# Kernel optimization log

Measured on AMD Instinct MI355X. Metric: run time of the kernel, lower is better.

## Reference

```python
import jax, jax.numpy as jnp
import numpy as np

WINDOW = 50


def setup_inputs() -> dict:
    key = jax.random.key(0)
    ks = jax.random.split(key, 7)
    B, N = 32, 32768
    hidden = 32
    x = jax.random.normal(ks[0], (B, N), dtype=jnp.float32)
    # torch Linear weights stored as [in, out] (already transposed)
    w1 = jax.random.normal(ks[1], (4, 2 * hidden), dtype=jnp.float32) * (1.0 / np.sqrt(4))
    b1 = jnp.zeros((2 * hidden,), dtype=jnp.float32)
    w2 = jax.random.normal(ks[2], (2 * hidden, hidden), dtype=jnp.float32) * (1.0 / np.sqrt(2 * hidden))
    b2 = jnp.zeros((hidden,), dtype=jnp.float32)
    w3 = jax.random.normal(ks[3], (hidden, 2), dtype=jnp.float32) * (1.0 / np.sqrt(hidden))
    b3 = jnp.zeros((2,), dtype=jnp.float32)
    return {"x": x, "w1": w1, "b1": b1, "w2": w2, "b2": b2, "w3": w3, "b3": b3}


def reference(x, w1, b1, w2, b2, w3, b3):
    W = WINDOW
    B, N = x.shape
    M = N - W + 1
    # windows: [B, M, W] via gather (same layout as torch.unfold)
    idx = jnp.arange(M)[:, None] + jnp.arange(W)[None, :]  # [M, W]
    windows = x[:, idx]  # [B, M, W]
    mean = windows.mean(axis=-1, keepdims=True)
    centered = windows - mean
    # torch .std() is unbiased (ddof=1)
    var = (centered ** 2).sum(axis=-1, keepdims=True) / (W - 1)
    std = jnp.sqrt(var) + 1e-6
    skew = (centered ** 3).mean(axis=-1, keepdims=True) / std ** 3
    kurt = (centered ** 4).mean(axis=-1, keepdims=True) / std ** 4
    stats = jnp.concatenate([mean, std, skew, kurt], axis=-1)  # [B, M, 4]
    h = jax.nn.relu(stats @ w1 + b1)
    h = jax.nn.relu(h @ w2 + b2)
    params = h @ w3 + b3  # [B, M, 2]
    gamma = params[:, :, 0:1]
    beta = params[:, :, 1:2]
    normalized = centered / std
    reprojected = normalized * gamma + beta  # [B, M, W]
    return reprojected[:, :, W // 2]  # [B, M]
```

## Files before the change

### kernel.cpp

```cpp
#include <hip/hip_runtime.h>
#include <hip/hip_bf16.h>
#include <math.h>

#define WINDOW 50
#define BPT 256

typedef __attribute__((ext_vector_type(8))) short short8;
typedef __attribute__((ext_vector_type(4))) float f32x4;
typedef unsigned int uint;

union U8 { uint4 u; short8 s; };
__device__ inline short8 as_s8(uint4 u) { U8 t; t.u = u; return t.s; }

__device__ inline uint pk2(float a, float b) {
    uint r;
    asm("v_cvt_pk_bf16_f32 %0, %1, %2" : "=v"(r) : "v"(a), "v"(b));
    return r;
}
__device__ inline float lo_f32(uint u) { return __uint_as_float(u << 16); }
__device__ inline float hi_f32(uint u) { return __uint_as_float(u & 0xffff0000u); }

#define LDS_FENCE() do { asm volatile("s_waitcnt lgkmcnt(0)" ::: "memory"); \
                         __builtin_amdgcn_sched_barrier(0); } while (0)

__global__ __launch_bounds__(256) void nsg_kernel(
    const float* __restrict__ x,
    const float* __restrict__ w1, const float* __restrict__ b1,
    const float* __restrict__ w2, const float* __restrict__ b2,
    const float* __restrict__ w3, const float* __restrict__ b3,
    float* __restrict__ out, int B, int N, int M, int tiles)
{
    __shared__ float s_x[BPT + WINDOW + 2];
    __shared__ f32x4 s_chunk[BPT + 40];
    __shared__ uint4 s_stat[4][64];
    __shared__ uint4 s_h1[4][128];
    __shared__ f32x4 s_h2[4][512];
    __shared__ f32x4 s_b1q[16];
    __shared__ f32x4 s_b2q[8];

    const int tid  = threadIdx.x;
    const int wv   = tid >> 6;
    const int wl   = tid & 63;
    const int l15  = wl & 15;
    const int g    = wl >> 4;
    const int tile = blockIdx.x % tiles;
    const int row  = blockIdx.x / tiles;
    const int m0   = tile * BPT;

    const float* xr = x + (size_t)row * N;
    for (int i = tid; i < BPT + WINDOW; i += 256) {
        int gg = m0 + i;
        s_x[i] = (gg < N) ? xr[gg] : 0.0f;
    }
    if (tid < 16) s_b1q[tid] = ((const f32x4*)b1)[tid];
    if (tid < 8)  s_b2q[tid] = ((const f32x4*)b2)[tid];

    short8 A1[4];
    #pragma unroll
    for (int nt = 0; nt < 4; ++nt) {
        int n = nt * 16 + l15;
        float a = w1[0 * 64 + n], b = w1[1 * 64 + n];
        float c = w1[2 * 64 + n], d = w1[3 * 64 + n];
        uint hab = pk2(a, b), hcd = pk2(c, d);
        float la = a - lo_f32(hab), lb = b - hi_f32(hab);
        float lc = c - lo_f32(hcd), ld = d - hi_f32(hcd);
        uint lab = pk2(la, lb), lcd = pk2(lc, ld);
        uint4 u;
        if (g == 0)      u = make_uint4(hab, hcd, hab, hcd);
        else if (g == 1) u = make_uint4(lab, lcd, lab, lcd);
        else             u = make_uint4(0, 0, 0, 0);
        A1[nt] = as_s8(u);
    }
    short8 A2h[2][2], A2l[2][2];
    #pragma unroll
    for (int mt = 0; mt < 2; ++mt) {
        int c = mt * 16 + l15;
        #pragma unroll
        for (int ks = 0; ks < 2; ++ks) {
            uint hu[4], lu[4];
            #pragma unroll
            for (int p = 0; p < 4; ++p) {
                int n = ks * 32 + g * 8 + 2 * p;
                float a = w2[n * 32 + c], b = w2[(n + 1) * 32 + c];
                uint h = pk2(a, b);
                float la = a - lo_f32(h), lb = b - hi_f32(h);
                hu[p] = h; lu[p] = pk2(la, lb);
            }
            A2h[mt][ks] = as_s8(make_uint4(hu[0], hu[1], hu[2], hu[3]));
            A2l[mt][ks] = as_s8(make_uint4(lu[0], lu[1], lu[2], lu[3]));
        }
    }
    __syncthreads();

    f32x4 myC;
    {
        float S1 = 0.f, S2 = 0.f, S3 = 0.f, S4 = 0.f;
        #pragma unroll
        for (int i = 0; i < 10; ++i) {
            float v = s_x[tid + i], v2 = v * v;
            S1 += v; S2 += v2; S3 = fmaf(v2, v, S3); S4 = fmaf(v2, v2, S4);
        }
        myC = f32x4{S1, S2, S3, S4};
        s_chunk[tid] = myC;
    }
    if (tid < 40) {
        float S1 = 0.f, S2 = 0.f, S3 = 0.f, S4 = 0.f;
        #pragma unroll
        for (int i = 0; i < 10; ++i) {
            float v = s_x[256 + tid + i], v2 = v * v;
            S1 += v; S2 += v2; S3 = fmaf(v2, v, S3); S4 = fmaf(v2, v2, S4);
        }
        s_chunk[256 + tid] = f32x4{S1, S2, S3, S4};
    }
    __syncthreads();

    f32x4 ca = s_chunk[tid + 10], cb = s_chunk[tid + 20];
    f32x4 cc = s_chunk[tid + 30], cd = s_chunk[tid + 40];
    float S1 = myC[0] + ca[0] + cb[0] + cc[0] + cd[0];
    float S2 = myC[1] + ca[1] + cb[1] + cc[1] + cd[1];
    float S3 = myC[2] + ca[2] + cb[2] + cc[2] + cd[2];
    float S4 = myC[3] + ca[3] + cb[3] + cc[3] + cd[3];

    const float invW = 1.0f / (float)WINDOW;
    float mean = S1 * invW;
    float mu2  = mean * mean;
    float c2m = S2 - (float)WINDOW * mu2;
    float c3m = S3 - 3.0f * mean * S2 + 2.0f * (float)WINDOW * mu2 * mean;
    float c4m = S4 - 4.0f * mean * S3 + 6.0f * mu2 * S2
                  - 3.0f * (float)WINDOW * mu2 * mu2;
    float var    = c2m * (1.0f / (float)(WINDOW - 1));
    float sd     = sqrtf(var) + 1e-6f;
    float inv_sd = 1.0f / sd;
    float inv_sd2 = inv_sd * inv_sd;
    float skew = c3m * invW * inv_sd2 * inv_sd;
    float kurt = c4m * invW * inv_sd2 * inv_sd2;
    float center = s_x[tid + 25];

    {
        uint h01 = pk2(mean, sd), h23 = pk2(skew, kurt);
        float ml = mean - lo_f32(h01), sl = sd   - hi_f32(h01);
        float kl = skew - lo_f32(h23), ul = kurt - hi_f32(h23);
        uint l01 = pk2(ml, sl), l23 = pk2(kl, ul);
        s_stat[wv][wl] = make_uint4(h01, h23, l01, l23);
    }
    LDS_FENCE();

    uint2* ph1 = (uint2*)&s_h1[wv][0];

    #pragma unroll
    for (int wt = 0; wt < 4; ++wt) {
        int w = wt * 16 + l15;
        short8 B1 = as_s8(s_stat[wv][w]);

        f32x4 C1[4];
        #pragma unroll
        for (int nt = 0; nt < 4; ++nt) C1[nt] = s_b1q[nt * 4 + g];
        #pragma unroll
        for (int nt = 0; nt < 4; ++nt)
            C1[nt] = __builtin_amdgcn_mfma_f32_16x16x32_bf16(A1[nt], B1, C1[nt], 0, 0, 0);

        #pragma unroll
        for (int nt = 0; nt < 4; ++nt) {
            uint p01 = pk2(fmaxf(C1[nt][0], 0.f), fmaxf(C1[nt][1], 0.f));
            uint p23 = pk2(fmaxf(C1[nt][2], 0.f), fmaxf(C1[nt][3], 0.f));
            int q = nt * 4 + g;
            uint2 t; t.x = p01; t.y = p23;
            ph1[(l15 * 16 + q) ^ ((l15 & 7) << 1)] = t;
        }
        LDS_FENCE();

        short8 B2k0 = as_s8(s_h1[wv][(l15 * 8 + 0 + g) ^ (l15 & 7)]);
        short8 B2k1 = as_s8(s_h1[wv][(l15 * 8 + 4 + g) ^ (l15 & 7)]);

        f32x4 C2[2];
        #pragma unroll
        for (int mt = 0; mt < 2; ++mt) C2[mt] = s_b2q[mt * 4 + g];
        #pragma unroll
        for (int mt = 0; mt < 2; ++mt) {
            C2[mt] = __builtin_amdgcn_mfma_f32_16x16x32_bf16(A2h[mt][0], B2k0, C2[mt], 0, 0, 0);
            C2[mt] = __builtin_amdgcn_mfma_f32_16x16x32_bf16(A2h[mt][1], B2k1, C2[mt], 0, 0, 0);
            C2[mt] = __builtin_amdgcn_mfma_f32_16x16x32_bf16(A2l[mt][0], B2k0, C2[mt], 0, 0, 0);
            C2[mt] = __builtin_amdgcn_mfma_f32_16x16x32_bf16(A2l[mt][1], B2k1, C2[mt], 0, 0, 0);
        }
        #pragma unroll
        for (int mt = 0; mt < 2; ++mt) {
            f32x4 hq;
            #pragma unroll
            for (int j = 0; j < 4; ++j) hq[j] = fmaxf(C2[mt][j], 0.f);
            s_h2[wv][(w * 8 + mt * 4 + g) ^ (w & 7)] = hq;
        }
    }
    LDS_FENCE();

    float gam = b3[0], bet = b3[1];
    #pragma unroll
    for (int q = 0; q < 8; ++q) {
        f32x4 h = s_h2[wv][(wl * 8 + q) ^ (wl & 7)];
        #pragma unroll
        for (int j = 0; j < 4; ++j) {
            int c = 16 * (q >> 2) + 4 * (q & 3) + j;
            gam = fmaf(h[j], w3[c * 2 + 0], gam);
            bet = fmaf(h[j], w3[c * 2 + 1], bet);
        }
    }

    const int m = m0 + tid;
    if (m < M)
        out[(size_t)row * M + m] = fmaf((center - mean) * inv_sd, gam, bet);
}

extern "C" void kernel_launch(void* const* d_in, const int* in_sizes, int n_in,
                              void* d_out, int out_size, void* d_ws, size_t ws_size,
                              hipStream_t stream) {
    const float* x  = (const float*)d_in[0];
    const float* w1 = (const float*)d_in[1];
    const float* b1 = (const float*)d_in[2];
    const float* w2 = (const float*)d_in[3];
    const float* b2 = (const float*)d_in[4];
    const float* w3 = (const float*)d_in[5];
    const float* b3 = (const float*)d_in[6];
    float* out = (float*)d_out;

    const int N = 32768;
    const int B = in_sizes[0] / N;
    const int M = N - WINDOW + 1;
    const int tiles = (M + BPT - 1) / BPT;

    dim3 grid(B * tiles), block(BPT);
    nsg_kernel<<<grid, block, 0, stream>>>(x, w1, b1, w2, b2, w3, b3,
                                           out, B, N, M, tiles);
}
```

Baseline: 35.63 us.

## Process two outputs per thread and fuse MLP layer-3 into MFMA epilogue

Each block now covers 512 output positions with 256 threads, so each thread handles two windows and the per-block weight-setup cost is amortized. The layer-1 bias is folded into the MFMA via a ones-row in B, and the layer-1 activation is split into hi/lo bf16 parts for extra precision. The A2 low part moves to LDS to cut register pressure, and launch bounds request 4 blocks per CU. The h2 store to LDS and the serial w3 dot product are replaced by an in-register reduction with cross-lane shuffles, at the cost of more MFMAs per tile and halving the grid size.

```diff
diff --git a/kernel.cpp b/kernel.cpp
--- a/kernel.cpp
+++ b/kernel.cpp
@@ -3,7 +3,6 @@
 #include <math.h>
 
 #define WINDOW 50
-#define BPT 256
 
 typedef __attribute__((ext_vector_type(8))) short short8;
 typedef __attribute__((ext_vector_type(4))) float f32x4;
@@ -20,58 +19,53 @@
 __device__ inline float lo_f32(uint u) { return __uint_as_float(u << 16); }
 __device__ inline float hi_f32(uint u) { return __uint_as_float(u & 0xffff0000u); }
 
-#define LDS_FENCE() do { asm volatile("s_waitcnt lgkmcnt(0)" ::: "memory"); \
-                         __builtin_amdgcn_sched_barrier(0); } while (0)
-
-__global__ __launch_bounds__(256) void nsg_kernel(
+__global__ __launch_bounds__(256, 4) void nsg_kernel(
     const float* __restrict__ x,
     const float* __restrict__ w1, const float* __restrict__ b1,
     const float* __restrict__ w2, const float* __restrict__ b2,
     const float* __restrict__ w3, const float* __restrict__ b3,
-    float* __restrict__ out, int B, int N, int M, int tiles)
+    float* __restrict__ out, int N, int M, int tiles)
 {
-    __shared__ float s_x[BPT + WINDOW + 2];
-    __shared__ f32x4 s_chunk[BPT + 40];
-    __shared__ uint4 s_stat[4][64];
-    __shared__ uint4 s_h1[4][128];
-    __shared__ f32x4 s_h2[4][512];
-    __shared__ f32x4 s_b1q[16];
-    __shared__ f32x4 s_b2q[8];
-
-    const int tid  = threadIdx.x;
-    const int wv   = tid >> 6;
-    const int wl   = tid & 63;
-    const int l15  = wl & 15;
-    const int g    = wl >> 4;
+    __shared__ float s_x[564];
+    __shared__ f32x4 s_buf[1088];
+    __shared__ uint4 s_a2l[4][64];
+    __shared__ uint4 s_stat[4][128];
+
+    const int tid = threadIdx.x;
+    const int wv  = tid >> 6;
+    const int wl  = tid & 63;
+    const int l15 = wl & 15;
+    const int g   = wl >> 4;
     const int tile = blockIdx.x % tiles;
     const int row  = blockIdx.x / tiles;
-    const int m0   = tile * BPT;
+    const int m0   = tile * 512;
 
     const float* xr = x + (size_t)row * N;
-    for (int i = tid; i < BPT + WINDOW; i += 256) {
+    for (int i = tid; i < 562; i += 256) {
         int gg = m0 + i;
         s_x[i] = (gg < N) ? xr[gg] : 0.0f;
     }
-    if (tid < 16) s_b1q[tid] = ((const f32x4*)b1)[tid];
-    if (tid < 8)  s_b2q[tid] = ((const f32x4*)b2)[tid];
 
     short8 A1[4];
     #pragma unroll
     for (int nt = 0; nt < 4; ++nt) {
         int n = nt * 16 + l15;
-        float a = w1[0 * 64 + n], b = w1[1 * 64 + n];
-        float c = w1[2 * 64 + n], d = w1[3 * 64 + n];
+        float a = w1[n], b = w1[64 + n], c = w1[128 + n], d = w1[192 + n];
         uint hab = pk2(a, b), hcd = pk2(c, d);
-        float la = a - lo_f32(hab), lb = b - hi_f32(hab);
-        float lc = c - lo_f32(hcd), ld = d - hi_f32(hcd);
-        uint lab = pk2(la, lb), lcd = pk2(lc, ld);
+        uint lab = pk2(a - lo_f32(hab), b - hi_f32(hab));
+        uint lcd = pk2(c - lo_f32(hcd), d - hi_f32(hcd));
+        float bb = b1[n];
+        uint bh = pk2(bb, 0.0f);
+        uint bpk = pk2(bb, bb - lo_f32(bh));
         uint4 u;
-        if (g == 0)      u = make_uint4(hab, hcd, hab, hcd);
-        else if (g == 1) u = make_uint4(lab, lcd, lab, lcd);
-        else             u = make_uint4(0, 0, 0, 0);
+        u.x = (g == 0) ? hab : (g == 1) ? lab : (g == 2) ? bpk : 0u;
+        u.y = (g == 0) ? hcd : (g == 1) ? lcd : 0u;
+        u.z = (g == 0) ? hab : (g == 1) ? lab : 0u;
+        u.w = (g == 0) ? hcd : (g == 1) ? lcd : 0u;
         A1[nt] = as_s8(u);
     }
-    short8 A2h[2][2], A2l[2][2];
+
+    uint4 A2h[2][2];
     #pragma unroll
     for (int mt = 0; mt < 2; ++mt) {
         int c = mt * 16 + l15;
@@ -83,130 +77,154 @@
                 int n = ks * 32 + g * 8 + 2 * p;
                 float a = w2[n * 32 + c], b = w2[(n + 1) * 32 + c];
                 uint h = pk2(a, b);
-                float la = a - lo_f32(h), lb = b - hi_f32(h);
-                hu[p] = h; lu[p] = pk2(la, lb);
+                hu[p] = h;
+                lu[p] = pk2(a - lo_f32(h), b - hi_f32(h));
             }
-            A2h[mt][ks] = as_s8(make_uint4(hu[0], hu[1], hu[2], hu[3]));
-            A2l[mt][ks] = as_s8(make_uint4(lu[0], lu[1], lu[2], lu[3]));
-        }
-    }
+            A2h[mt][ks] = make_uint4(hu[0], hu[1], hu[2], hu[3]);
+            if (wv == 0) s_a2l[mt * 2 + ks][wl] = make_uint4(lu[0], lu[1], lu[2], lu[3]);
+        }
+    }
+
+    f32x4 b2r[2];
+    #pragma unroll
+    for (int mt = 0; mt < 2; ++mt)
+        b2r[mt] = *(const f32x4*)(b2 + 16 * mt + 4 * g);
+    float2 w3r[8];
+    #pragma unroll
+    for (int mt = 0; mt < 2; ++mt)
+        #pragma unroll
+        for (int j = 0; j < 4; ++j)
+            w3r[mt * 4 + j] = *(const float2*)(w3 + (16 * mt + 4 * g + j) * 2);
+    const float b3g = b3[0], b3b = b3[1];
+
     __syncthreads();
 
-    f32x4 myC;
-    {
+    f32x4* s_chunk = s_buf;
+    f32x4 myC[2];
+    #pragma unroll
+    for (int s = 0; s < 2; ++s) {
+        int t = tid + 256 * s;
         float S1 = 0.f, S2 = 0.f, S3 = 0.f, S4 = 0.f;
         #pragma unroll
         for (int i = 0; i < 10; ++i) {
-            float v = s_x[tid + i], v2 = v * v;
+            float v = s_x[t + i], v2 = v * v;
             S1 += v; S2 += v2; S3 = fmaf(v2, v, S3); S4 = fmaf(v2, v2, S4);
         }
-        myC = f32x4{S1, S2, S3, S4};
-        s_chunk[tid] = myC;
+        myC[s] = f32x4{S1, S2, S3, S4};
+        s_chunk[t] = myC[s];
     }
     if (tid < 40) {
+        int t = tid + 512;
         float S1 = 0.f, S2 = 0.f, S3 = 0.f, S4 = 0.f;
         #pragma unroll
         for (int i = 0; i < 10; ++i) {
-            float v = s_x[256 + tid + i], v2 = v * v;
+            float v = s_x[t + i], v2 = v * v;
             S1 += v; S2 += v2; S3 = fmaf(v2, v, S3); S4 = fmaf(v2, v2, S4);
         }
-        s_chunk[256 + tid] = f32x4{S1, S2, S3, S4};
+        s_chunk[t] = f32x4{S1, S2, S3, S4};
     }
     __syncthreads();
 
-    f32x4 ca = s_chunk[tid + 10], cb = s_chunk[tid + 20];
-    f32x4 cc = s_chunk[tid + 30], cd = s_chunk[tid + 40];
-    float S1 = myC[0] + ca[0] + cb[0] + cc[0] + cd[0];
-    float S2 = myC[1] + ca[1] + cb[1] + cc[1] + cd[1];
-    float S3 = myC[2] + ca[2] + cb[2] + cc[2] + cd[2];
-    float S4 = myC[3] + ca[3] + cb[3] + cc[3] + cd[3];
-
-    const float invW = 1.0f / (float)WINDOW;
-    float mean = S1 * invW;
-    float mu2  = mean * mean;
-    float c2m = S2 - (float)WINDOW * mu2;
-    float c3m = S3 - 3.0f * mean * S2 + 2.0f * (float)WINDOW * mu2 * mean;
-    float c4m = S4 - 4.0f * mean * S3 + 6.0f * mu2 * S2
-                  - 3.0f * (float)WINDOW * mu2 * mu2;
-    float var    = c2m * (1.0f / (float)(WINDOW - 1));
-    float sd     = sqrtf(var) + 1e-6f;
-    float inv_sd = 1.0f / sd;
-    float inv_sd2 = inv_sd * inv_sd;
-    float skew = c3m * invW * inv_sd2 * inv_sd;
-    float kurt = c4m * invW * inv_sd2 * inv_sd2;
-    float center = s_x[tid + 25];
-
-    {
+    float nrm[2];
+    #pragma unroll
+    for (int s = 0; s < 2; ++s) {
+        int t = tid + 256 * s;
+        f32x4 ca = s_chunk[t + 10], cb = s_chunk[t + 20];
+        f32x4 cc = s_chunk[t + 30], cd = s_chunk[t + 40];
+        float S1 = myC[s][0] + ca[0] + cb[0] + cc[0] + cd[0];
+        float S2 = myC[s][1] + ca[1] + cb[1] + cc[1] + cd[1];
+        float S3 = myC[s][2] + ca[2] + cb[2] + cc[2] + cd[2];
+        float S4 = myC[s][3] + ca[3] + cb[3] + cc[3] + cd[3];
+        const float invW = 1.0f / (float)WINDOW;
+        float mean = S1 * invW;
+        float mu2  = mean * mean;
+        float c2m = S2 - (float)WINDOW * mu2;
+        float c3m = S3 - 3.0f * mean * S2 + 2.0f * (float)WINDOW * mu2 * mean;
+        float c4m = S4 - 4.0f * mean * S3 + 6.0f * mu2 * S2
+                      - 3.0f * (float)WINDOW * mu2 * mu2;
+        float var    = c2m * (1.0f / (float)(WINDOW - 1));
+        float sd     = sqrtf(var) + 1e-6f;
+        float inv_sd = 1.0f / sd;
+        float inv_sd2 = inv_sd * inv_sd;
+        float skew = c3m * invW * inv_sd2 * inv_sd;
+        float kurt = c4m * invW * inv_sd2 * inv_sd2;
         uint h01 = pk2(mean, sd), h23 = pk2(skew, kurt);
-        float ml = mean - lo_f32(h01), sl = sd   - hi_f32(h01);
-        float kl = skew - lo_f32(h23), ul = kurt - hi_f32(h23);
-        uint l01 = pk2(ml, sl), l23 = pk2(kl, ul);
-        s_stat[wv][wl] = make_uint4(h01, h23, l01, l23);
-    }
-    LDS_FENCE();
-
-    uint2* ph1 = (uint2*)&s_h1[wv][0];
-
-    #pragma unroll
-    for (int wt = 0; wt < 4; ++wt) {
-        int w = wt * 16 + l15;
-        short8 B1 = as_s8(s_stat[wv][w]);
-
-        f32x4 C1[4];
-        #pragma unroll
-        for (int nt = 0; nt < 4; ++nt) C1[nt] = s_b1q[nt * 4 + g];
-        #pragma unroll
-        for (int nt = 0; nt < 4; ++nt)
-            C1[nt] = __builtin_amdgcn_mfma_f32_16x16x32_bf16(A1[nt], B1, C1[nt], 0, 0, 0);
+        uint l01 = pk2(mean - lo_f32(h01), sd - hi_f32(h01));
+        uint l23 = pk2(skew - lo_f32(h23), kurt - hi_f32(h23));
+        s_stat[wv][s * 64 + wl] = make_uint4(h01, h23, l01, l23);
+        nrm[s] = (s_x[t + 25] - mean) * inv_sd;
+    }
+    __syncthreads();
+
+    uint* h1b = (uint*)(s_buf + wv * 272);
+    const uint K2 = (g == 2) ? 0x3F803F80u : 0u;
+    const bool gHi = (g >= 2);
+    float ga[2] = {0.f, 0.f}, be[2] = {0.f, 0.f};
+
+    #pragma unroll
+    for (int q = 0; q < 8; ++q) {
+        const int s = q >> 2, sub = q & 3;
+        uint4 st = s_stat[wv][s * 64 + sub * 16 + l15];
+        uint4 bq;
+        bq.x = gHi ? K2 : st.x;
+        bq.y = gHi ? 0u : st.y;
+        bq.z = gHi ? 0u : st.z;
+        bq.w = gHi ? 0u : st.w;
+        short8 B1 = as_s8(bq);
 
         #pragma unroll
         for (int nt = 0; nt < 4; ++nt) {
-            uint p01 = pk2(fmaxf(C1[nt][0], 0.f), fmaxf(C1[nt][1], 0.f));
-            uint p23 = pk2(fmaxf(C1[nt][2], 0.f), fmaxf(C1[nt][3], 0.f));
-            int q = nt * 4 + g;
-            uint2 t; t.x = p01; t.y = p23;
-            ph1[(l15 * 16 + q) ^ ((l15 & 7) << 1)] = t;
-        }
-        LDS_FENCE();
-
-        short8 B2k0 = as_s8(s_h1[wv][(l15 * 8 + 0 + g) ^ (l15 & 7)]);
-        short8 B2k1 = as_s8(s_h1[wv][(l15 * 8 + 4 + g) ^ (l15 & 7)]);
-
-        f32x4 C2[2];
-        #pragma unroll
-        for (int mt = 0; mt < 2; ++mt) C2[mt] = s_b2q[mt * 4 + g];
+            f32x4 c1 = f32x4{0.f, 0.f, 0.f, 0.f};
+            c1 = __builtin_amdgcn_mfma_f32_16x16x32_bf16(A1[nt], B1, c1, 0, 0, 0);
+            float r0 = fmaxf(c1[0], 0.f), r1 = fmaxf(c1[1], 0.f);
+            float r2 = fmaxf(c1[2], 0.f), r3 = fmaxf(c1[3], 0.f);
+            uint h01 = pk2(r0, r1), h23 = pk2(r2, r3);
+            uint q01 = pk2(r0 - lo_f32(h01), r1 - hi_f32(h01));
+            uint q23 = pk2(r2 - lo_f32(h23), r3 - hi_f32(h23));
+            int d = l15 * 68 + 8 * nt + 2 * g;
+            *(uint2*)&h1b[d]      = make_uint2(h01, h23);
+            *(uint2*)&h1b[d + 32] = make_uint2(q01, q23);
+        }
+        __builtin_amdgcn_wave_barrier();
+
+        short8 Bh0 = as_s8(*(uint4*)&h1b[l15 * 68 +  0 + 4 * g]);
+        short8 Bh1 = as_s8(*(uint4*)&h1b[l15 * 68 + 16 + 4 * g]);
+        short8 Bl0 = as_s8(*(uint4*)&h1b[l15 * 68 + 32 + 4 * g]);
+        short8 Bl1 = as_s8(*(uint4*)&h1b[l15 * 68 + 48 + 4 * g]);
+
+        float pg = 0.f, pb = 0.f;
         #pragma unroll
         for (int mt = 0; mt < 2; ++mt) {
-            C2[mt] = __builtin_amdgcn_mfma_f32_16x16x32_bf16(A2h[mt][0], B2k0, C2[mt], 0, 0, 0);
-            C2[mt] = __builtin_amdgcn_mfma_f32_16x16x32_bf16(A2h[mt][1], B2k1, C2[mt], 0, 0, 0);
-            C2[mt] = __builtin_amdgcn_mfma_f32_16x16x32_bf16(A2l[mt][0], B2k0, C2[mt], 0, 0, 0);
-            C2[mt] = __builtin_amdgcn_mfma_f32_16x16x32_bf16(A2l[mt][1], B2k1, C2[mt], 0, 0, 0);
-        }
-        #pragma unroll
-        for (int mt = 0; mt < 2; ++mt) {
-            f32x4 hq;
+            short8 a2l0 = as_s8(s_a2l[mt * 2 + 0][wl]);
+            short8 a2l1 = as_s8(s_a2l[mt * 2 + 1][wl]);
+            f32x4 c2 = b2r[mt];
+            c2 = __builtin_amdgcn_mfma_f32_16x16x32_bf16(as_s8(A2h[mt][0]), Bh0, c2, 0, 0, 0);
+            c2 = __builtin_amdgcn_mfma_f32_16x16x32_bf16(as_s8(A2h[mt][1]), Bh1, c2, 0, 0, 0);
+            c2 = __builtin_amdgcn_mfma_f32_16x16x32_bf16(as_s8(A2h[mt][0]), Bl0, c2, 0, 0, 0);
+            c2 = __builtin_amdgcn_mfma_f32_16x16x32_bf16(as_s8(A2h[mt][1]), Bl1, c2, 0, 0, 0);
+            c2 = __builtin_amdgcn_mfma_f32_16x16x32_bf16(a2l0, Bh0, c2, 0, 0, 0);
+            c2 = __builtin_amdgcn_mfma_f32_16x16x32_bf16(a2l1, Bh1, c2, 0, 0, 0);
             #pragma unroll
-            for (int j = 0; j < 4; ++j) hq[j] = fmaxf(C2[mt][j], 0.f);
-            s_h2[wv][(w * 8 + mt * 4 + g) ^ (w & 7)] = hq;
-        }
-    }
-    LDS_FENCE();
-
-    float gam = b3[0], bet = b3[1];
-    #pragma unroll
-    for (int q = 0; q < 8; ++q) {
-        f32x4 h = s_h2[wv][(wl * 8 + q) ^ (wl & 7)];
-        #pragma unroll
-        for (int j = 0; j < 4; ++j) {
-            int c = 16 * (q >> 2) + 4 * (q & 3) + j;
-            gam = fmaf(h[j], w3[c * 2 + 0], gam);
-            bet = fmaf(h[j], w3[c * 2 + 1], bet);
-        }
-    }
-
-    const int m = m0 + tid;
-    if (m < M)
-        out[(size_t)row * M + m] = fmaf((center - mean) * inv_sd, gam, bet);
+            for (int j = 0; j < 4; ++j) {
+                float P = fmaxf(c2[j], 0.f);
+                float2 w = w3r[mt * 4 + j];
+                pg = fmaf(P, w.x, pg);
+                pb = fmaf(P, w.y, pb);
+            }
+        }
+        pg += __shfl_xor(pg, 16);
+        pb += __shfl_xor(pb, 16);
+        pg += __shfl_xor(pg, 32);
+        pb += __shfl_xor(pb, 32);
+        if (g == sub) { ga[s] = pg; be[s] = pb; }
+    }
+
+    #pragma unroll
+    for (int s = 0; s < 2; ++s) {
+        int m = m0 + tid + 256 * s;
+        if (m < M)
+            out[(size_t)row * M + m] = fmaf(nrm[s], ga[s] + b3g, be[s] + b3b);
+    }
 }
 
 extern "C" void kernel_launch(void* const* d_in, const int* in_sizes, int n_in,
@@ -224,9 +242,9 @@
     const int N = 32768;
     const int B = in_sizes[0] / N;
     const int M = N - WINDOW + 1;
-    const int tiles = (M + BPT - 1) / BPT;
-
-    dim3 grid(B * tiles), block(BPT);
+    const int tiles = (M + 511) / 512;
+
+    dim3 grid(B * tiles), block(256);
     nsg_kernel<<<grid, block, 0, stream>>>(x, w1, b1, w2, b2, w3, b3,
-                                           out, B, N, M, tiles);
+                                           out, N, M, tiles);
 }
```

After: 34.51 us. 1.03x faster.
